# Kernel optimization log

Hardware: AMD Instinct MI355X
Metric: run time of the kernel (lower is better)

## Reference

```python
import jax, jax.numpy as jnp
import numpy as np

N = 32768       # batch of states
DQ = 8          # q_ndim (dof_ndim)
A = 4           # action_dim
H = 1024        # hidden_size


def setup_inputs() -> dict:
    key = jax.random.key(0)
    ks = jax.random.split(key, 16)

    def lin(kw, kb, fan_out, fan_in, zero_bias=False):
        s = 1.0 / np.sqrt(fan_in)
        W = jax.random.normal(kw, (fan_out, fan_in), dtype=jnp.float32) * s
        b = jnp.zeros((fan_out,), jnp.float32) if zero_bias else \
            jax.random.normal(kb, (fan_out,), dtype=jnp.float32) * s
        return W, b

    W1, b1 = lin(ks[0], ks[1], H, 2 * DQ)            # h_net layer 1
    W2, b2 = lin(ks[2], ks[3], H, H)                 # h_net layer 2
    Wh, bh = lin(ks[4], ks[5], 1, H)                 # h_net head -> scalar H(z)
    Wf1, bf1 = lin(ks[6], ks[7], H, 2 * DQ + A)      # flex_net layer 1
    Wf2, bf2 = lin(ks[8], ks[9], H, H)               # flex_net layer 2
    Wff, bff = lin(ks[10], ks[11], 2 * DQ, H)        # flex_net head -> 2*q_ndim
    Wp, bp = lin(ks[12], ks[13], A, 2 * DQ)          # control policy (detached)

    return {
        "t": jnp.zeros((), jnp.float32),
        "z": jax.random.normal(ks[14], (N, 2 * DQ), dtype=jnp.float32),
        "W1": W1, "b1": b1, "W2": W2, "b2": b2, "Wh": Wh, "bh": bh,
        "Wf1": Wf1, "bf1": bf1, "Wf2": Wf2, "bf2": bf2, "Wff": Wff, "bff": bff,
        "Wp": Wp, "bp": bp,
    }


def reference(t, z, W1, b1, W2, b2, Wh, bh,
              Wf1, bf1, Wf2, bf2, Wff, bff, Wp, bp):
    # control input, detached as in the torch forward (u = policy(t, z).detach())
    u = jax.lax.stop_gradient(jnp.tanh(z @ Wp.T + bp))  # [N, A]

    # ---- H-net forward, saving tanh' at each activation (the `sps` list) ----
    # angular_dims=() -> CosSin is the identity, so h_net[0](z) = z.
    a1 = z @ W1.T + b1          # [N, H]
    h1 = jnp.tanh(a1)
    s0 = 1.0 - h1 * h1          # d tanh / d a1   (sps[0])
    a2 = h1 @ W2.T + b2         # [N, H]
    h2 = jnp.tanh(a2)
    s1 = 1.0 - h2 * h2          # d tanh / d a2   (sps[1])

    # dH = grad_z sum(h_net(z)), with gradients flowing (create_graph=True)
    def H_sum(zz):
        hh = jnp.tanh(zz @ W1.T + b1)
        hh = jnp.tanh(hh @ W2.T + b2)
        return jnp.sum(hh @ Wh.T + bh)

    dH = jax.grad(H_sum)(z)     # [N, 2*DQ]

    # ---- flex-net with skip term modulated by reversed tanh' maps ----
    zu = jnp.concatenate([z, u], axis=-1)       # [N, 2*DQ + A]
    f1 = zu @ Wf1.T + bf1
    g1 = jnp.tanh(f1) + f1 * s1                 # idx = 1 -> sps[1]
    f2 = g1 @ Wf2.T + bf2
    g2 = jnp.tanh(f2) + f2 * s0                 # idx = 0 -> sps[0]
    out = g2 @ Wff.T + bff                      # [N, 2*DQ]

    # D = jacobian of CosSin = identity per batch row (angular_dims=()), so
    # bmm(out[:,None,:], D).squeeze(1) == out.

    # dz_dt = J @ (out + dH):  J([top; bot]) = [bot; -top]
    s = out + dH
    return jnp.concatenate([s[:, DQ:], -s[:, :DQ]], axis=-1)  # [N, 2*DQ]
```

## Files before the change

kernel.cpp:

```cpp
#include <hip/hip_runtime.h>
#include <hip/hip_bf16.h>

typedef __hip_bfloat16 bf16;
typedef __attribute__((ext_vector_type(8))) short short8;
typedef __attribute__((ext_vector_type(4))) short s16x4;
typedef __attribute__((ext_vector_type(4))) float f32x4;

__device__ __forceinline__ bf16 f2b(float f) { return __float2bfloat16(f); }
__device__ __forceinline__ short bfbits(float f) {
  union { float f; unsigned u; } x; x.f = f;
  unsigned r = x.u + 0x7fff + ((x.u >> 16) & 1);
  return (short)(r >> 16);
}
__device__ __forceinline__ float tanh_fast(float x) {
  float t = __expf(-2.f * fabsf(x));
  float r = (1.f - t) * __builtin_amdgcn_rcpf(1.f + t);
  return copysignf(r, x);
}

#define GLOAD_LDS16(gp, lp) __builtin_amdgcn_global_load_lds( \
    (const __attribute__((address_space(1))) void*)(gp), \
    (__attribute__((address_space(3))) void*)(lp), 16, 0, 0)
#define SBAR() __builtin_amdgcn_s_barrier()
#define WAITV(n) do { asm volatile("s_waitcnt vmcnt(" #n ")" ::: "memory"); \
                      __builtin_amdgcn_sched_barrier(0); } while (0)
#define LGKM0() do { asm volatile("s_waitcnt lgkmcnt(0)" ::: "memory"); \
                     __builtin_amdgcn_sched_barrier(0); } while (0)

__global__ __launch_bounds__(256) void prep(
    const float* __restrict__ W2, const float* __restrict__ Wf2,
    const float* __restrict__ W1, const float* __restrict__ Wff,
    bf16* __restrict__ W2bf, bf16* __restrict__ W2Tbf,
    bf16* __restrict__ Wf2bf, bf16* __restrict__ W1n,
    bf16* __restrict__ Wffn)
{
  __shared__ float T[32][33];
  const int tid = threadIdx.x, bx = blockIdx.x;
  const int tx = bx & 31, ty = bx >> 5;
  const int r = tid >> 3, c4 = (tid & 7) * 4;
  const long ibase = (long)(ty * 32 + r) * 1024 + tx * 32 + c4;

  f32x4 v = *(const f32x4*)(W2 + ibase);
  f32x4 vf = *(const f32x4*)(Wf2 + ibase);
  s16x4 sv, sf;
  #pragma unroll
  for (int j = 0; j < 4; ++j) {
    sv[j] = bfbits(v[j]); sf[j] = bfbits(vf[j]);
    T[r][c4 + j] = v[j];
  }
  *(s16x4*)(W2bf + ibase) = sv;
  *(s16x4*)(Wf2bf + ibase) = sf;
  __syncthreads();
  const int oc = tid >> 3, or4 = (tid & 7) * 4;
  s16x4 st;
  #pragma unroll
  for (int j = 0; j < 4; ++j) st[j] = bfbits(T[or4 + j][oc]);
  *(s16x4*)(W2Tbf + (long)(tx * 32 + oc) * 1024 + ty * 32 + or4) = st;

  if (bx < 32) {
    #pragma unroll
    for (int rep = 0; rep < 2; ++rep) {
      int i = bx * 512 + rep * 256 + tid;
      int rr = i >> 10, cc = i & 1023;
      W1n[i] = f2b(W1[cc * 16 + rr]);
      Wffn[i] = f2b(Wff[i]);
    }
  }
}

__global__ __launch_bounds__(256) void k1(
    const float* __restrict__ z, const float* __restrict__ W1,
    const float* __restrict__ b1, const float* __restrict__ Wp,
    const float* __restrict__ bp, const float* __restrict__ Wf1,
    const float* __restrict__ bf1v,
    bf16* __restrict__ h1, bf16* __restrict__ f1out, long grow0)
{
  __shared__ float zs[32][16];
  __shared__ float us[32][4];
  const int tid = threadIdx.x;
  const long r0 = (long)blockIdx.x * 32;
  for (int i = tid; i < 512; i += 256) {
    int r = i >> 4, c = i & 15;
    zs[r][c] = z[(grow0 + r0 + r) * 16 + c];
  }
  __syncthreads();
  if (tid < 128) {
    int r = tid >> 2, a = tid & 3;
    float acc = bp[a];
    #pragma unroll
    for (int k = 0; k < 16; ++k) acc = fmaf(zs[r][k], Wp[a * 16 + k], acc);
    us[r][a] = tanh_fast(acc);
  }
  __syncthreads();
  #pragma unroll
  for (int jj = 0; jj < 4; ++jj) {
    const int c = tid + jj * 256;
    {
      float w[16];
      #pragma unroll
      for (int k = 0; k < 16; ++k) w[k] = W1[c * 16 + k];
      const float bc = b1[c];
      for (int r = 0; r < 32; ++r) {
        float a = bc;
        #pragma unroll
        for (int k = 0; k < 16; ++k) a = fmaf(zs[r][k], w[k], a);
        h1[(r0 + r) * 1024 + c] = f2b(tanh_fast(a));
      }
    }
    {
      float wf[20];
      #pragma unroll
      for (int k = 0; k < 20; ++k) wf[k] = Wf1[c * 20 + k];
      const float bfc = bf1v[c];
      for (int r = 0; r < 32; ++r) {
        float f = bfc;
        #pragma unroll
        for (int k = 0; k < 16; ++k) f = fmaf(zs[r][k], wf[k], f);
        #pragma unroll
        for (int a = 0; a < 4; ++a) f = fmaf(us[r][a], wf[16 + a], f);
        f1out[(r0 + r) * 1024 + c] = f2b(f);
      }
    }
  }
}

template<int EPI>
__global__ __launch_bounds__(512, 2) void gemm_k(
    const bf16* __restrict__ A, const bf16* __restrict__ Bp,
    const float* __restrict__ bias, const float* __restrict__ Whv,
    const bf16* __restrict__ h1,
    bf16* O1, bf16* __restrict__ O2,
    const bf16* __restrict__ Wn, float* __restrict__ Pp, int ckRows)
{
  __shared__ __align__(16) char smem[131072];
  const int tid = threadIdx.x;
  const int lane = tid & 63, wid = tid >> 6;
  const int wr = wid >> 2, wc = wid & 3;
  const int fr = lane & 15, kg = lane >> 4;
  const long row0 = (long)blockIdx.x * 256;
  const int col0 = blockIdx.y * 256;

  const int sr0 = tid >> 2;
  const int sk0 = ((tid & 3) ^ ((tid >> 3) & 3)) * 8;
  const int swr = (fr >> 1) & 3;

  const bf16* gA0 = A + (row0 + sr0) * 1024 + sk0;
  const bf16* gB0 = Bp + ((long)col0 + sr0) * 1024 + sk0;
  const int rdA = (wr * 128 + fr) * 32 + (kg ^ swr) * 8;
  const int rdB = (wc * 64 + fr) * 32 + (kg ^ swr) * 8;

  f32x4 acc[8][4] = {};

  auto stage = [&](int b, int k0) {
    bf16* as = (bf16*)smem + b * 8192;
    bf16* bs = (bf16*)smem + 32768 + b * 8192;
    GLOAD_LDS16(gA0 + k0, as + tid * 8);
    GLOAD_LDS16(gA0 + 128 * 1024 + k0, as + 4096 + tid * 8);
    GLOAD_LDS16(gB0 + k0, bs + tid * 8);
    GLOAD_LDS16(gB0 + 128 * 1024 + k0, bs + 4096 + tid * 8);
  };

  stage(0, 0); stage(1, 32); stage(2, 64);
  WAITV(8); SBAR();

  #pragma unroll
  for (int kt = 0; kt < 32; ++kt) {
    const bf16* as = (const bf16*)smem + (kt & 3) * 8192;
    const bf16* bs = (const bf16*)smem + 32768 + (kt & 3) * 8192;
    const int k3 = (kt + 3) * 32;
    bf16* sa = (bf16*)smem + ((kt + 3) & 3) * 8192;
    bf16* sb = (bf16*)smem + 32768 + ((kt + 3) & 3) * 8192;

    short8 af[8], bfr[4];
    #pragma unroll
    for (int m = 0; m < 4; ++m)
      af[m] = *(const short8*)(as + rdA + m * 512);
    #pragma unroll
    for (int n = 0; n < 4; ++n)
      bfr[n] = *(const short8*)(bs + rdB + n * 512);
    if (kt + 3 < 32) {
      GLOAD_LDS16(gA0 + k3, sa + tid * 8);
      GLOAD_LDS16(gA0 + 128 * 1024 + k3, sa + 4096 + tid * 8);
    }
    SBAR(); LGKM0();
    __builtin_amdgcn_s_setprio(1);
    #pragma unroll
    for (int m = 0; m < 4; ++m)
      #pragma unroll
      for (int n = 0; n < 4; ++n)
        acc[m][n] = __builtin_amdgcn_mfma_f32_16x16x32_bf16(af[m], bfr[n], acc[m][n], 0, 0, 0);
    __builtin_amdgcn_s_setprio(0);
    SBAR();
    #pragma unroll
    for (int m = 4; m < 8; ++m)
      af[m] = *(const short8*)(as + rdA + m * 512);
    if (kt + 3 < 32) {
      GLOAD_LDS16(gB0 + k3, sb + tid * 8);
      GLOAD_LDS16(gB0 + 128 * 1024 + k3, sb + 4096 + tid * 8);
    }
    SBAR(); LGKM0();
    __builtin_amdgcn_s_setprio(1);
    #pragma unroll
    for (int m = 4; m < 8; ++m)
      #pragma unroll
      for (int n = 0; n < 4; ++n)
        acc[m][n] = __builtin_amdgcn_mfma_f32_16x16x32_bf16(af[m], bfr[n], acc[m][n], 0, 0, 0);
    __builtin_amdgcn_s_setprio(0);
    if (kt < 29)       WAITV(8);
    else if (kt == 29) WAITV(4);
    else if (kt == 30) WAITV(0);
    if (kt < 31) SBAR();
  }

  if (EPI == 0) {
    #pragma unroll
    for (int m = 0; m < 8; ++m) {
      const long gr0 = row0 + wr * 128 + m * 16 + kg * 4;
      #pragma unroll
      for (int n = 0; n < 4; ++n) {
        const int gc = col0 + wc * 64 + n * 16 + fr;
        const float b2c = bias[gc], whc = Whv[gc];
        f32x4 v = acc[m][n];
        #pragma unroll
        for (int j = 0; j < 4; ++j) {
          const long idx = (gr0 + j) * 1024 + gc;
          float h = tanh_fast(v[j] + b2c);
          float s1v = 1.f - h * h;
          float f = __bfloat162float(((const bf16*)O1)[idx]);
          O2[idx] = f2b(s1v * whc);
          O1[idx] = f2b(tanh_fast(f) + f * s1v);
        }
      }
    }
  } else {
    __syncthreads();
    bf16* Ot = (bf16*)smem;
    f32x4 pacc[2] = {};
    #pragma unroll
    for (int ph = 0; ph < 2; ++ph) {
      if ((wc >> 1) == ph) {
        #pragma unroll
        for (int m = 0; m < 8; ++m) {
          const int rl0 = wr * 128 + m * 16 + kg * 4;
          const long gr0 = row0 + rl0;
          #pragma unroll
          for (int n = 0; n < 4; ++n) {
            const int cl = (wc & 1) * 64 + n * 16 + fr;
            const int gc = col0 + ph * 128 + cl;
            f32x4 v = acc[m][n];
            #pragma unroll
            for (int j = 0; j < 4; ++j) {
              const long idx = (gr0 + j) * 1024 + gc;
              float x = v[j], g;
              if (EPI == 1) {
                float hh = __bfloat162float(h1[idx]);
                g = x * (1.f - hh * hh);
              } else {
                float f = x + bias[gc];
                float hh = __bfloat162float(h1[idx]);
                g = tanh_fast(f) + f * (1.f - hh * hh);
              }
              Ot[(rl0 + j) * 136 + cl] = f2b(g);
            }
          }
        }
      }
      __syncthreads();
      #pragma unroll
      for (int sub = 0; sub < 2; ++sub) {
        const int rl0 = wid * 32 + sub * 16;
        #pragma unroll
        for (int ks = 0; ks < 4; ++ks) {
          short8 afrag = *(const short8*)(Ot + (rl0 + fr) * 136 + ks * 32 + kg * 8);
          short8 bfrag = *(const short8*)(Wn + fr * 1024 + col0 + ph * 128 + ks * 32 + kg * 8);
          pacc[sub] = __builtin_amdgcn_mfma_f32_16x16x32_bf16(afrag, bfrag, pacc[sub], 0, 0, 0);
        }
      }
      if (ph == 0) __syncthreads();
    }
    #pragma unroll
    for (int sub = 0; sub < 2; ++sub) {
      const int rl0 = wid * 32 + sub * 16;
      #pragma unroll
      for (int j = 0; j < 4; ++j)
        Pp[(((long)blockIdx.y) * ckRows + row0 + rl0 + kg * 4 + j) * 16 + fr] = pacc[sub][j];
    }
  }
}

__global__ __launch_bounds__(256) void k7(
    const float* __restrict__ Pp0, const float* __restrict__ Pp1,
    const float* __restrict__ bff, float* __restrict__ out,
    long grow0, int ckRows)
{
  int i = blockIdx.x * 256 + threadIdx.x;
  int r = i >> 4, j = i & 15, jp = (j + 8) & 15;
  float s = bff[jp];
  #pragma unroll
  for (int cb = 0; cb < 4; ++cb) {
    long o = ((long)cb * ckRows + r) * 16 + jp;
    s += Pp0[o] + Pp1[o];
  }
  out[(grow0 + r) * 16 + j] = (j < 8) ? s : -s;
}

extern "C" void kernel_launch(void* const* d_in, const int* in_sizes, int n_in,
                              void* d_out, int out_size, void* d_ws, size_t ws_size,
                              hipStream_t stream) {
  const float* z   = (const float*)d_in[1];
  const float* W1  = (const float*)d_in[2];
  const float* b1  = (const float*)d_in[3];
  const float* W2  = (const float*)d_in[4];
  const float* b2  = (const float*)d_in[5];
  const float* Wh  = (const float*)d_in[6];
  const float* Wf1 = (const float*)d_in[8];
  const float* bf1 = (const float*)d_in[9];
  const float* Wf2 = (const float*)d_in[10];
  const float* bf2 = (const float*)d_in[11];
  const float* Wff = (const float*)d_in[12];
  const float* bff = (const float*)d_in[13];
  const float* Wp  = (const float*)d_in[14];
  const float* bp  = (const float*)d_in[15];
  float* out = (float*)d_out;
  const int N = in_sizes[1] / 16;

  char* p = (char*)d_ws;
  auto alloc = [&](size_t bytes) {
    char* q = p; p += (bytes + 255) & ~(size_t)255; return q;
  };
  bf16* W2bf  = (bf16*)alloc(1024 * 1024 * 2);
  bf16* W2Tbf = (bf16*)alloc(1024 * 1024 * 2);
  bf16* Wf2bf = (bf16*)alloc(1024 * 1024 * 2);
  bf16* W1n   = (bf16*)alloc(16 * 1024 * 2);
  bf16* Wffn  = (bf16*)alloc(16 * 1024 * 2);
  size_t wbytes = (size_t)(p - (char*)d_ws);

  int CK = N;
  while (CK > 256 && wbytes + (size_t)CK * 6656 > ws_size) CK >>= 1;
  bf16* actA = (bf16*)alloc((size_t)CK * 2048);
  bf16* actB = (bf16*)alloc((size_t)CK * 2048);
  bf16* actD = (bf16*)alloc((size_t)CK * 2048);
  float* Pp0 = (float*)alloc((size_t)CK * 4 * 16 * 4);
  float* Pp1 = (float*)alloc((size_t)CK * 4 * 16 * 4);

  prep<<<1024, 256, 0, stream>>>(W2, Wf2, W1, Wff, W2bf, W2Tbf, Wf2bf, W1n, Wffn);

  const dim3 ggrid(CK / 256, 4);
  for (long r0 = 0; r0 < N; r0 += CK) {
    k1<<<CK / 32, 256, 0, stream>>>(z, W1, b1, Wp, bp, Wf1, bf1, actA, actD, r0);
    gemm_k<0><<<ggrid, 512, 0, stream>>>(
        actA, W2bf, b2, Wh, nullptr, actD, actB, nullptr, nullptr, CK);
    gemm_k<1><<<ggrid, 512, 0, stream>>>(
        actB, W2Tbf, nullptr, nullptr, actA, nullptr, nullptr, W1n, Pp0, CK);
    gemm_k<2><<<ggrid, 512, 0, stream>>>(
        actD, Wf2bf, bf2, nullptr, actA, nullptr, nullptr, Wffn, Pp1, CK);
    k7<<<CK / 16, 256, 0, stream>>>(Pp0, Pp1, bff, out, r0, CK);
  }
}
```

Measured before the change: 351.2 us.

## Restructure GEMM mainloop to double-buffered 64-wide K chunks with half-stage prefetch

Replaces the 4-stage ring of 32-wide K tiles with two 64-wide K buffers, each split into two 32-wide halves. Global-to-LDS prefetch of the next chunk is spread across four sub-steps, so each half is issued while MFMAs run on the current chunk. The loop now runs 16 iterations with unroll 2 and waits at vmcnt(4). The explicit __syncthreads before the second epilogue is removed and replaced by the final loop barrier. This aims to cut barrier and wait overhead per K step and reduce register pressure from the af array, at the cost of shallower prefetch depth and possible exposed memory latency.

```diff
diff --git a/kernel.cpp b/kernel.cpp
--- a/kernel.cpp
+++ b/kernel.cpp
@@ -140,48 +140,50 @@
   const long row0 = (long)blockIdx.x * 256;
   const int col0 = blockIdx.y * 256;
 
-  const int sr0 = tid >> 2;
   const int sk0 = ((tid & 3) ^ ((tid >> 3) & 3)) * 8;
   const int swr = (fr >> 1) & 3;
 
-  const bf16* gA0 = A + (row0 + sr0) * 1024 + sk0;
-  const bf16* gB0 = Bp + ((long)col0 + sr0) * 1024 + sk0;
+  const bf16* gA0 = A + (row0 + (tid >> 2)) * 1024 + sk0;
+  const bf16* gB0 = Bp + ((long)col0 + (tid >> 2)) * 1024 + sk0;
   const int rdA = (wr * 128 + fr) * 32 + (kg ^ swr) * 8;
   const int rdB = (wc * 64 + fr) * 32 + (kg ^ swr) * 8;
 
+  bf16* const Ae = (bf16*)smem;
+  bf16* const Be = (bf16*)smem + 32768;
+
   f32x4 acc[8][4] = {};
 
-  auto stage = [&](int b, int k0) {
-    bf16* as = (bf16*)smem + b * 8192;
-    bf16* bs = (bf16*)smem + 32768 + b * 8192;
-    GLOAD_LDS16(gA0 + k0, as + tid * 8);
-    GLOAD_LDS16(gA0 + 128 * 1024 + k0, as + 4096 + tid * 8);
-    GLOAD_LDS16(gB0 + k0, bs + tid * 8);
-    GLOAD_LDS16(gB0 + 128 * 1024 + k0, bs + 4096 + tid * 8);
+  auto stageA = [&](int c1, int k0, int h) {
+    bf16* d = Ae + c1 * 16384 + h * 8192;
+    GLOAD_LDS16(gA0 + k0 + h * 32, d + tid * 8);
+    GLOAD_LDS16(gA0 + 128 * 1024 + k0 + h * 32, d + 4096 + tid * 8);
   };
-
-  stage(0, 0); stage(1, 32); stage(2, 64);
-  WAITV(8); SBAR();
-
-  #pragma unroll
-  for (int kt = 0; kt < 32; ++kt) {
-    const bf16* as = (const bf16*)smem + (kt & 3) * 8192;
-    const bf16* bs = (const bf16*)smem + 32768 + (kt & 3) * 8192;
-    const int k3 = (kt + 3) * 32;
-    bf16* sa = (bf16*)smem + ((kt + 3) & 3) * 8192;
-    bf16* sb = (bf16*)smem + 32768 + ((kt + 3) & 3) * 8192;
-
-    short8 af[8], bfr[4];
+  auto stageB = [&](int c1, int k0, int h) {
+    bf16* d = Be + c1 * 16384 + h * 8192;
+    GLOAD_LDS16(gB0 + k0 + h * 32, d + tid * 8);
+    GLOAD_LDS16(gB0 + 128 * 1024 + k0 + h * 32, d + 4096 + tid * 8);
+  };
+
+  stageA(0, 0, 0); stageB(0, 0, 0); stageA(0, 0, 1); stageB(0, 0, 1);
+  WAITV(4);
+  SBAR();
+
+  #pragma unroll 2
+  for (int kt = 0; kt < 16; ++kt) {
+    const int c = kt & 1;
+    const int c1 = c ^ 1;
+    const int k0 = (kt + 1) * 64;
+    const bf16* as = Ae + c * 16384;
+    const bf16* bs = Be + c * 16384;
+    short8 af[4], bfr[4];
+
     #pragma unroll
     for (int m = 0; m < 4; ++m)
       af[m] = *(const short8*)(as + rdA + m * 512);
     #pragma unroll
     for (int n = 0; n < 4; ++n)
       bfr[n] = *(const short8*)(bs + rdB + n * 512);
-    if (kt + 3 < 32) {
-      GLOAD_LDS16(gA0 + k3, sa + tid * 8);
-      GLOAD_LDS16(gA0 + 128 * 1024 + k3, sa + 4096 + tid * 8);
-    }
+    if (kt < 15) stageA(c1, k0, 0);
     SBAR(); LGKM0();
     __builtin_amdgcn_s_setprio(1);
     #pragma unroll
@@ -191,25 +193,53 @@
         acc[m][n] = __builtin_amdgcn_mfma_f32_16x16x32_bf16(af[m], bfr[n], acc[m][n], 0, 0, 0);
     __builtin_amdgcn_s_setprio(0);
     SBAR();
-    #pragma unroll
-    for (int m = 4; m < 8; ++m)
-      af[m] = *(const short8*)(as + rdA + m * 512);
-    if (kt + 3 < 32) {
-      GLOAD_LDS16(gB0 + k3, sb + tid * 8);
-      GLOAD_LDS16(gB0 + 128 * 1024 + k3, sb + 4096 + tid * 8);
-    }
+
+    #pragma unroll
+    for (int m = 0; m < 4; ++m)
+      af[m] = *(const short8*)(as + rdA + (m + 4) * 512);
+    if (kt < 15) stageB(c1, k0, 0);
     SBAR(); LGKM0();
     __builtin_amdgcn_s_setprio(1);
     #pragma unroll
-    for (int m = 4; m < 8; ++m)
+    for (int m = 0; m < 4; ++m)
+      #pragma unroll
+      for (int n = 0; n < 4; ++n)
+        acc[m + 4][n] = __builtin_amdgcn_mfma_f32_16x16x32_bf16(af[m], bfr[n], acc[m + 4][n], 0, 0, 0);
+    __builtin_amdgcn_s_setprio(0);
+    if (kt < 15) WAITV(4); else WAITV(0);
+    SBAR();
+
+    #pragma unroll
+    for (int m = 0; m < 4; ++m)
+      af[m] = *(const short8*)(as + 8192 + rdA + m * 512);
+    #pragma unroll
+    for (int n = 0; n < 4; ++n)
+      bfr[n] = *(const short8*)(bs + 8192 + rdB + n * 512);
+    if (kt < 15) stageA(c1, k0, 1);
+    SBAR(); LGKM0();
+    __builtin_amdgcn_s_setprio(1);
+    #pragma unroll
+    for (int m = 0; m < 4; ++m)
       #pragma unroll
       for (int n = 0; n < 4; ++n)
         acc[m][n] = __builtin_amdgcn_mfma_f32_16x16x32_bf16(af[m], bfr[n], acc[m][n], 0, 0, 0);
     __builtin_amdgcn_s_setprio(0);
-    if (kt < 29)       WAITV(8);
-    else if (kt == 29) WAITV(4);
-    else if (kt == 30) WAITV(0);
-    if (kt < 31) SBAR();
+    SBAR();
+
+    #pragma unroll
+    for (int m = 0; m < 4; ++m)
+      af[m] = *(const short8*)(as + 8192 + rdA + (m + 4) * 512);
+    if (kt < 15) stageB(c1, k0, 1);
+    SBAR(); LGKM0();
+    __builtin_amdgcn_s_setprio(1);
+    #pragma unroll
+    for (int m = 0; m < 4; ++m)
+      #pragma unroll
+      for (int n = 0; n < 4; ++n)
+        acc[m + 4][n] = __builtin_amdgcn_mfma_f32_16x16x32_bf16(af[m], bfr[n], acc[m + 4][n], 0, 0, 0);
+    __builtin_amdgcn_s_setprio(0);
+    if (kt < 15) WAITV(4); else WAITV(0);
+    SBAR();
   }
 
   if (EPI == 0) {
@@ -233,7 +263,6 @@
       }
     }
   } else {
-    __syncthreads();
     bf16* Ot = (bf16*)smem;
     f32x4 pacc[2] = {};
     #pragma unroll
```

New measurement: 351.5 us. No clear change (+0.1%).
